# Optimization experiments

Measured on AMD Instinct MI355X. Metric: run time of the kernel, lower is better.

## Reference

```python
import jax, jax.numpy as jnp
import numpy as np
from jax import lax

N_CTX = 65536   # total contexts
B = 512         # samples (segments for attention pooling)
E = 128         # emb_size
H = 128         # rnn_size // 2 (per direction)
T = 9           # path length
SUB_V = 50000
NODE_V = 512
DEC = 320
OUT = 10000
L = N_CTX * 5   # total subtoken occurrences per side


def setup_inputs() -> dict:
    key = jax.random.key(0)
    ks = jax.random.split(key, 24)
    s = 0.05
    d = {}
    d["ll_subtokens"] = jax.random.randint(ks[0], (L,), 0, SUB_V, dtype=jnp.int32)
    d["ll_indices"] = jnp.sort(jax.random.randint(ks[1], (L,), 0, N_CTX, dtype=jnp.int32))
    d["rl_subtokens"] = jax.random.randint(ks[2], (L,), 0, SUB_V, dtype=jnp.int32)
    d["rl_indices"] = jnp.sort(jax.random.randint(ks[3], (L,), 0, N_CTX, dtype=jnp.int32))
    d["paths"] = jax.random.randint(ks[4], (N_CTX, T), 0, NODE_V, dtype=jnp.int32)
    d["indices"] = jnp.sort(jax.random.randint(ks[5], (N_CTX,), 0, B, dtype=jnp.int32))
    d["subtoken_emb"] = jax.random.normal(ks[6], (SUB_V, E), jnp.float32) * s
    d["node_emb"] = jax.random.normal(ks[7], (NODE_V, E), jnp.float32) * s
    d["w_ih_f"] = jax.random.normal(ks[8], (4 * H, E), jnp.float32) * s
    d["w_hh_f"] = jax.random.normal(ks[9], (4 * H, H), jnp.float32) * s
    d["b_ih_f"] = jax.random.normal(ks[10], (4 * H,), jnp.float32) * s
    d["b_hh_f"] = jax.random.normal(ks[11], (4 * H,), jnp.float32) * s
    d["w_ih_b"] = jax.random.normal(ks[12], (4 * H, E), jnp.float32) * s
    d["w_hh_b"] = jax.random.normal(ks[13], (4 * H, H), jnp.float32) * s
    d["b_ih_b"] = jax.random.normal(ks[14], (4 * H,), jnp.float32) * s
    d["b_hh_b"] = jax.random.normal(ks[15], (4 * H,), jnp.float32) * s
    d["fc_w"] = jax.random.normal(ks[16], (DEC, 2 * E + 2 * H), jnp.float32) * s
    d["a"] = jax.random.uniform(ks[17], (DEC,), jnp.float32)  # nn.init.uniform_
    d["out_w"] = jax.random.normal(ks[18], (OUT, DEC), jnp.float32) * s
    d["out_b"] = jax.random.normal(ks[19], (OUT,), jnp.float32) * s
    return d


def _lstm_last_hidden(x, w_ih, w_hh, b_ih, b_hh):
    """x: [T, N, E] -> final hidden state [N, H]. PyTorch gate order i,f,g,o."""
    n = x.shape[1]
    bias = b_ih + b_hh

    def step(carry, xt):
        h, c = carry
        g = xt @ w_ih.T + h @ w_hh.T + bias          # [N, 4H]
        i, f, gg, o = jnp.split(g, 4, axis=-1)
        c = jax.nn.sigmoid(f) * c + jax.nn.sigmoid(i) * jnp.tanh(gg)
        h = jax.nn.sigmoid(o) * jnp.tanh(c)
        return (h, c), None

    init = (jnp.zeros((n, H), x.dtype), jnp.zeros((n, H), x.dtype))
    (h, _), _ = lax.scan(step, init, x)
    return h


def reference(ll_subtokens, ll_indices, rl_subtokens, rl_indices, paths, indices,
              subtoken_emb, node_emb,
              w_ih_f, w_hh_f, b_ih_f, b_hh_f,
              w_ih_b, w_hh_b, b_ih_b, b_hh_b,
              fc_w, a, out_w, out_b):
    # scatter-add subtoken embeddings into per-context leaf embeddings
    ll_emb = jax.ops.segment_sum(subtoken_emb[ll_subtokens], ll_indices, num_segments=N_CTX)
    rl_emb = jax.ops.segment_sum(subtoken_emb[rl_subtokens], rl_indices, num_segments=N_CTX)

    # bidirectional LSTM over path node embeddings; final hidden states
    x = jnp.swapaxes(node_emb[paths], 0, 1)          # [T, N_CTX, E]
    h_f = _lstm_last_hidden(x, w_ih_f, w_hh_f, b_ih_f, b_hh_f)
    h_b = _lstm_last_hidden(x[::-1], w_ih_b, w_hh_b, b_ih_b, b_hh_b)
    path_agg = jnp.concatenate([h_f, h_b], axis=1)   # [N_CTX, 2H]

    ctx = jnp.concatenate([ll_emb, path_agg, rl_emb], axis=1)  # [N_CTX, 2E+2H]
    # dropout is identity in eval mode
    ctx = jnp.tanh(ctx @ fc_w.T)                     # [N_CTX, DEC]

    # segment softmax attention over contexts within each sample
    score = ctx @ a                                  # [N_CTX]
    m = jax.ops.segment_max(score, indices, num_segments=B)
    e = jnp.exp(score - m[indices])
    s = jax.ops.segment_sum(e, indices, num_segments=B)
    w = e / s[indices]
    v = jax.ops.segment_sum(ctx * w[:, None], indices, num_segments=B)  # [B, DEC]

    return v @ out_w.T + out_b                       # [B, OUT]
```

## Files before the change

### kernel.cpp

```cpp
#include <hip/hip_runtime.h>


#define N_CTX_ 65536
#define B_     512
#define E_     128
#define H_     128
#define T_     9
#define DEC_   320
#define OUT_   10000
#define L_     (N_CTX_*5)

typedef __bf16 bf16;
typedef __bf16 bf16x8 __attribute__((ext_vector_type(8)));
typedef __bf16 bf16x4 __attribute__((ext_vector_type(4)));
typedef float  f32x4  __attribute__((ext_vector_type(4)));
typedef float  f32x2  __attribute__((ext_vector_type(2)));
typedef __fp16 f16x2  __attribute__((ext_vector_type(2)));

__device__ __forceinline__ float fast_sig(float x){
  float e = __builtin_amdgcn_exp2f(x * -1.4426950408889634f);
  return __builtin_amdgcn_rcpf(1.0f + e);
}
__device__ __forceinline__ float fast_tanh(float x){
  float e = __builtin_amdgcn_exp2f(x * -2.8853900817779268f);
  return 2.0f * __builtin_amdgcn_rcpf(1.0f + e) - 1.0f;
}
__device__ __forceinline__ int lbound(const int* __restrict__ a, int n, int key){
  int lo = 0, hi = n;
  while (lo < hi){ int mid = (lo + hi) >> 1; if (a[mid] < key) lo = mid + 1; else hi = mid; }
  return lo;
}

__device__ __forceinline__ f32x2 pkmul(f32x2 a, f32x2 b){
  f32x2 d; asm("v_pk_mul_f32 %0, %1, %2" : "=v"(d) : "v"(a), "v"(b)); return d;
}
__device__ __forceinline__ f32x2 pkfma(f32x2 a, f32x2 b, f32x2 c){
  f32x2 d; asm("v_pk_fma_f32 %0, %1, %2, %3" : "=v"(d) : "v"(a), "v"(b), "v"(c)); return d;
}
__device__ __forceinline__ f32x2 pkfma_s(f32x2 a, f32x2 b, f32x2 c){
  f32x2 d; asm("v_pk_fma_f32 %0, %1, %2, %3" : "=v"(d) : "v"(a), "v"(b), "s"(c)); return d;
}

__device__ __forceinline__ f32x4 sig4(f32x4 x){
  const f32x2 S3v = {-2.1081349e-4f, -2.1081349e-4f};
  const f32x2 S2  = { 2.0833333e-3f,  2.0833333e-3f};
  const f32x2 S1  = {-2.0833333e-2f, -2.0833333e-2f};
  const f32x2 S0  = { 0.25f, 0.25f};
  const f32x2 HF  = { 0.5f, 0.5f};
  f32x2 xl = {x[0], x[1]}, xh = {x[2], x[3]};
  f32x2 tl = pkmul(xl, xl), th = pkmul(xh, xh);
  f32x2 pl = pkfma_s(tl, S3v, S2), ph = pkfma_s(th, S3v, S2);
  pl = pkfma_s(pl, tl, S1); ph = pkfma_s(ph, th, S1);
  pl = pkfma_s(pl, tl, S0); ph = pkfma_s(ph, th, S0);
  pl = pkfma_s(xl, pl, HF); ph = pkfma_s(xh, ph, HF);
  return f32x4{pl[0], pl[1], ph[0], ph[1]};
}
__device__ __forceinline__ f32x4 tanh4(f32x4 x){
  const f32x2 C4v = { 0.021869489f,  0.021869489f};
  const f32x2 C3  = {-0.053968254f, -0.053968254f};
  const f32x2 C2  = { 0.13333333f,   0.13333333f};
  const f32x2 C1  = {-0.33333333f,  -0.33333333f};
  const f32x2 C0  = { 1.0f, 1.0f};
  f32x2 xl = {x[0], x[1]}, xh = {x[2], x[3]};
  f32x2 tl = pkmul(xl, xl), th = pkmul(xh, xh);
  f32x2 pl = pkfma_s(tl, C4v, C3), ph = pkfma_s(th, C4v, C3);
  pl = pkfma_s(pl, tl, C2); ph = pkfma_s(ph, th, C2);
  pl = pkfma_s(pl, tl, C1); ph = pkfma_s(ph, th, C1);
  pl = pkfma_s(pl, tl, C0); ph = pkfma_s(ph, th, C0);
  pl = pkmul(xl, pl); ph = pkmul(xh, ph);
  return f32x4{pl[0], pl[1], ph[0], ph[1]};
}
__device__ __forceinline__ f32x4 mul4(f32x4 a, f32x4 b){
  f32x2 l = pkmul(f32x2{a[0],a[1]}, f32x2{b[0],b[1]});
  f32x2 h = pkmul(f32x2{a[2],a[3]}, f32x2{b[2],b[3]});
  return f32x4{l[0], l[1], h[0], h[1]};
}
__device__ __forceinline__ f32x4 fma4(f32x4 a, f32x4 b, f32x4 c){
  f32x2 l = pkfma(f32x2{a[0],a[1]}, f32x2{b[0],b[1]}, f32x2{c[0],c[1]});
  f32x2 h = pkfma(f32x2{a[2],a[3]}, f32x2{b[2],b[3]}, f32x2{c[2],c[3]});
  return f32x4{l[0], l[1], h[0], h[1]};
}

__global__ __launch_bounds__(256) void k_pf(
    const float* __restrict__ nemb,
    const float* __restrict__ wihf, const float* __restrict__ bihf, const float* __restrict__ bhhf,
    const float* __restrict__ wihb, const float* __restrict__ bihb, const float* __restrict__ bhhb,
    bf16* __restrict__ Pf4, bf16* __restrict__ Pb4)
{
  const int node = blockIdx.x, dir = blockIdx.y;
  const float* wih = dir ? wihb : wihf;
  const float* bi  = dir ? bihb : bihf;
  const float* bh  = dir ? bhhb : bhhf;
  bf16* P = dir ? Pb4 : Pf4;
  __shared__ float x[128];
  if (threadIdx.x < 128) x[threadIdx.x] = nemb[node*128 + threadIdx.x];
  __syncthreads();
  const float4* x4 = (const float4*)x;
  #pragma unroll
  for (int jj = 0; jj < 2; ++jj){
    int j = threadIdx.x + jj*256;
    const float4* w4 = (const float4*)(wih + j*128);
    float acc = bi[j] + bh[j];
    #pragma unroll
    for (int k = 0; k < 32; ++k){
      float4 a = w4[k], b = x4[k];
      acc += a.x*b.x + a.y*b.y + a.z*b.z + a.w*b.w;
    }
    int gate = j >> 7, n = (j >> 4) & 7, cc = j & 15;
    int slot = (gate < 2) ? (1 - gate) : gate;
    P[(((size_t)node*16 + cc) << 5) + slot*8 + n] = (bf16)acc;
  }
}

__global__ __launch_bounds__(256) void k_cvt(
    const float* __restrict__ fcw, const float* __restrict__ outw,
    const float* __restrict__ whhf, const float* __restrict__ whhb_,
    const float* __restrict__ semb,
    bf16* __restrict__ fcwb, bf16* __restrict__ outwb,
    bf16* __restrict__ whhfb, bf16* __restrict__ whhbb, bf16* __restrict__ sembb)
{
  size_t i = ((size_t)blockIdx.x*256 + threadIdx.x) * 4;
  const float* src; bf16* dst; size_t off;
  if      (i < 163840)              { src = fcw;   dst = fcwb;  off = i; }
  else if (i < 163840+3200000)      { src = outw;  dst = outwb; off = i - 163840; }
  else if (i < 163840+3200000+65536){ src = whhf;  dst = whhfb; off = i - 3363840; }
  else if (i < 3429376+65536)       { src = whhb_; dst = whhbb; off = i - 3429376; }
  else                              { src = semb;  dst = sembb; off = i - 3494912; }
  float4 v = *(const float4*)(src + off);
  bf16x4 o; o[0]=(bf16)v.x; o[1]=(bf16)v.y; o[2]=(bf16)v.z; o[3]=(bf16)v.w;
  *(bf16x4*)(dst + off) = o;
}

__global__ __launch_bounds__(256) void k_bounds(
    const int* __restrict__ lli, const int* __restrict__ rli,
    int* __restrict__ startL, int* __restrict__ startR)
{
  const int* si = blockIdx.y ? rli : lli;
  int* st = blockIdx.y ? startR : startL;
  int p = blockIdx.x*256 + threadIdx.x;
  if (p > L_) return;
  int cur = (p < L_) ? si[p] : N_CTX_;
  int prv = (p > 0) ? si[p-1] : -1;
  for (int c = prv + 1; c <= cur; ++c) st[c] = p;
}

__global__ __launch_bounds__(256) void k_leaf(
    const int* __restrict__ lls, const int* __restrict__ rls,
    const int* __restrict__ startL, const int* __restrict__ startR,
    const bf16* __restrict__ sembb, bf16* __restrict__ ctx_in)
{
  int u = blockIdx.x*4 + (threadIdx.x >> 6);
  int lane = threadIdx.x & 63;
  int ctx = u >> 1, side = u & 1;
  const int* st  = side ? rls    : lls;
  const int* stt = side ? startR : startL;
  int a = stt[ctx], b = stt[ctx+1];
  float a0 = 0.f, a1 = 0.f;
  for (int p = a; p < b; ++p){
    unsigned w = *(const unsigned*)&sembb[(size_t)st[p]*128 + lane*2];
    a0 += __uint_as_float(w << 16);
    a1 += __uint_as_float(w & 0xffff0000u);
  }
  bf16 r0 = (bf16)a0, r1 = (bf16)a1;
  unsigned pk = ((unsigned)*(unsigned short*)&r1 << 16) | *(unsigned short*)&r0;
  *(unsigned*)&ctx_in[(size_t)ctx*512 + (side ? 384 : 0) + lane*2] = pk;
}

__device__ __forceinline__ void slot_mfma(
    int slot, const bf16* __restrict__ whh, int lo4, int hi4,
    const bf16x8 afr[][4], const int nd[][4], const bf16* __restrict__ P4,
    f32x4 acc[][8])
{
  bf16x8 pv[2][4];
  #pragma unroll
  for (int m = 0; m < 2; ++m)
  #pragma unroll
  for (int r = 0; r < 4; ++r)
    pv[m][r] = *(const bf16x8*)(P4 + (((size_t)nd[m][r]*16 + lo4) << 5) + slot*8);
  #pragma unroll
  for (int m = 0; m < 2; ++m)
  #pragma unroll
  for (int n = 0; n < 8; ++n){
    f32x4 a;
    #pragma unroll
    for (int r = 0; r < 4; ++r){
      unsigned w = ((const unsigned*)&pv[m][r])[n >> 1];
      a[r] = (n & 1) ? __uint_as_float(w & 0xffff0000u) : __uint_as_float(w << 16);
    }
    acc[m][n] = a;
  }
  #pragma unroll
  for (int n = 0; n < 8; ++n)
  #pragma unroll
  for (int kk = 0; kk < 4; ++kk){
    int row = slot*128 + n*16 + lo4;
    bf16x8 bfr = *(const bf16x8*)&whh[row*128 + (((kk*4 + hi4) ^ (row & 15)) << 3)];
    acc[0][n] = __builtin_amdgcn_mfma_f32_16x16x32_bf16(afr[0][kk], bfr, acc[0][n], 0,0,0);
    acc[1][n] = __builtin_amdgcn_mfma_f32_16x16x32_bf16(afr[1][kk], bfr, acc[1][n], 0,0,0);
  }
}

__global__ __launch_bounds__(512, 2) void k_lstm(
    const int* __restrict__ paths,
    const bf16* __restrict__ whhfb, const bf16* __restrict__ whhbb,
    const bf16* __restrict__ Pf4,   const bf16* __restrict__ Pb4,
    bf16* __restrict__ ctx_in)
{
  const int dir = blockIdx.y;
  const bf16* __restrict__ whhg = dir ? whhbb : whhfb;
  const bf16* __restrict__ P4   = dir ? Pb4   : Pf4;
  __shared__ __align__(16) bf16 whh[512*128];
  __shared__ __align__(16) bf16 hlds[8*16*64];
  const int tid = threadIdx.x;
  const int lane = tid & 63, wid = tid >> 6;
  const int lo4 = lane & 15, hi4 = lane >> 4;

  #pragma unroll
  for (int it = 0; it < 16; ++it){
    int i = tid + it*512;
    int srow = i >> 4, c16 = i & 15;
    int gate = srow >> 7, rr = srow & 127;
    int slot = (gate < 2) ? (1 - gate) : gate;
    int drow = slot*128 + rr;
    *(bf16x8*)&whh[drow*128 + ((c16 ^ (drow & 15)) << 3)] =
        *(const bf16x8*)&whhg[srow*128 + c16*8];
  }
  __syncthreads();

  bf16* __restrict__ hbuf = &hlds[wid*1024];
  const int ctx0 = blockIdx.x*256 + wid*32;

  f32x4 c[2][8];
  bf16x8 afr[2][4];
  #pragma unroll
  for (int m = 0; m < 2; ++m){
    #pragma unroll
    for (int n = 0; n < 8; ++n) c[m][n] = f32x4{0.f,0.f,0.f,0.f};
    #pragma unroll
    for (int kk = 0; kk < 4; ++kk) afr[m][kk] = bf16x8{};
  }

  int nd[2][4];
  {
    int tt0 = dir ? (T_-1) : 0;
    #pragma unroll
    for (int m = 0; m < 2; ++m)
    #pragma unroll
    for (int r = 0; r < 4; ++r)
      nd[m][r] = paths[(ctx0 + m*16 + hi4*4 + r)*T_ + tt0];
  }

  #pragma unroll 1
  for (int s = 0; s < T_; ++s){
    int ndn[2][4];
    if (s + 1 < T_){
      int ttn = dir ? (T_-2-s) : (s+1);
      #pragma unroll
      for (int m = 0; m < 2; ++m)
      #pragma unroll
      for (int r = 0; r < 4; ++r)
        ndn[m][r] = paths[(ctx0 + m*16 + hi4*4 + r)*T_ + ttn];
    }
    f32x4 acc[2][8];
    f16x2 iact[2][8][2];

    slot_mfma(0, whh, lo4, hi4, afr, nd, P4, acc);
    #pragma unroll
    for (int m = 0; m < 2; ++m)
    #pragma unroll
    for (int n = 0; n < 8; ++n) c[m][n] = mul4(sig4(acc[m][n]), c[m][n]);

    slot_mfma(1, whh, lo4, hi4, afr, nd, P4, acc);
    #pragma unroll
    for (int m = 0; m < 2; ++m)
    #pragma unroll
    for (int n = 0; n < 8; ++n){
      f32x4 sv = sig4(acc[m][n]);
      iact[m][n][0] = __builtin_amdgcn_cvt_pkrtz(sv[0], sv[1]);
      iact[m][n][1] = __builtin_amdgcn_cvt_pkrtz(sv[2], sv[3]);
    }

    slot_mfma(2, whh, lo4, hi4, afr, nd, P4, acc);
    #pragma unroll
    for (int m = 0; m < 2; ++m)
    #pragma unroll
    for (int n = 0; n < 8; ++n){
      f32x4 ia = {(float)iact[m][n][0][0], (float)iact[m][n][0][1],
                  (float)iact[m][n][1][0], (float)iact[m][n][1][1]};
      c[m][n] = fma4(ia, tanh4(acc[m][n]), c[m][n]);
    }

    slot_mfma(3, whh, lo4, hi4, afr, nd, P4, acc);
    #pragma unroll
    for (int mp = 0; mp < 2; ++mp){
      f32x4 hv[8];
      #pragma unroll
      for (int n = 0; n < 8; ++n) hv[n] = mul4(sig4(acc[mp][n]), tanh4(c[mp][n]));
      if (s < T_-1){
        #pragma unroll
        for (int np = 0; np < 2; ++np){
          #pragma unroll
          for (int n2 = 0; n2 < 4; ++n2)
          #pragma unroll
          for (int r = 0; r < 4; ++r){
            int row = hi4*4 + r;
            int colb = n2*16 + lo4;
            hbuf[row*64 + (((colb >> 3) ^ (row & 7)) << 3) + (colb & 7)] =
                (bf16)hv[np*4 + n2][r];
          }
          #pragma unroll
          for (int kk2 = 0; kk2 < 2; ++kk2)
            afr[mp][np*2 + kk2] =
                *(const bf16x8*)&hbuf[lo4*64 + (((kk2*4 + hi4) ^ (lo4 & 7)) << 3)];
        }
      } else {
        #pragma unroll
        for (int n = 0; n < 8; ++n)
        #pragma unroll
        for (int r = 0; r < 4; ++r)
          ctx_in[(size_t)(ctx0 + mp*16 + hi4*4 + r)*512 + 128 + dir*128 + n*16 + lo4] =
              (bf16)hv[n][r];
      }
    }
    #pragma unroll
    for (int m = 0; m < 2; ++m)
    #pragma unroll
    for (int r = 0; r < 4; ++r) nd[m][r] = ndn[m][r];
  }
}

__global__ __launch_bounds__(256, 2) void k_fc(
    const bf16* __restrict__ ctx_in, const bf16* __restrict__ fcwb,
    const float* __restrict__ avec, bf16* __restrict__ ctxb, float* __restrict__ score)
{
  __shared__ __align__(16) bf16 bsl[320*32];
  const int tid = threadIdx.x, lane = tid & 63, wid = tid >> 6;
  const int lo4 = lane & 15, hi4 = lane >> 4;
  const int rowbase = blockIdx.x*64 + wid*16;
  bf16x8 afr[16];
  #pragma unroll
  for (int kk = 0; kk < 16; ++kk)
    afr[kk] = *(const bf16x8*)&ctx_in[(size_t)(rowbase + lo4)*512 + kk*32 + hi4*8];
  f32x4 acc[20];
  #pragma unroll
  for (int nt = 0; nt < 20; ++nt) acc[nt] = f32x4{0.f,0.f,0.f,0.f};
  #pragma unroll
  for (int kk = 0; kk < 16; ++kk){
    __syncthreads();
    #pragma unroll
    for (int i = 0; i < 5; ++i){
      int cc = tid + i*256;
      int row = cc >> 2, cg = (cc & 3) << 3;
      *(bf16x8*)&bsl[row*32 + (cg ^ ((row & 3) << 3))] =
          *(const bf16x8*)&fcwb[(size_t)row*512 + kk*32 + cg];
    }
    __syncthreads();
    #pragma unroll
    for (int nt = 0; nt < 20; ++nt){
      int row = nt*16 + lo4;
      bf16x8 b = *(const bf16x8*)&bsl[row*32 + ((hi4*8) ^ ((row & 3) << 3))];
      acc[nt] = __builtin_amdgcn_mfma_f32_16x16x32_bf16(afr[kk], b, acc[nt], 0,0,0);
    }
  }
  float sc[4] = {0.f,0.f,0.f,0.f};
  #pragma unroll
  for (int nt = 0; nt < 20; ++nt){
    float av = avec[nt*16 + lo4];
    #pragma unroll
    for (int r = 0; r < 4; ++r){
      float t = fast_tanh(acc[nt][r]);
      ctxb[(size_t)(rowbase + hi4*4 + r)*320 + nt*16 + lo4] = (bf16)t;
      sc[r] += t * av;
    }
  }
  #pragma unroll
  for (int r = 0; r < 4; ++r){
    #pragma unroll
    for (int o = 1; o < 16; o <<= 1) sc[r] += __shfl_xor(sc[r], o, 64);
  }
  if (lo4 == 0){
    #pragma unroll
    for (int r = 0; r < 4; ++r) score[rowbase + hi4*4 + r] = sc[r];
  }
}

__global__ __launch_bounds__(320) void k_attn(
    const int* __restrict__ sidx, const float* __restrict__ score,
    const bf16* __restrict__ ctxb, bf16* __restrict__ vb)
{
  const int b = blockIdx.x, tid = threadIdx.x;
  const int lane = tid & 63, wid = tid >> 6;
  const int lo = lbound(sidx, N_CTX_, b);
  const int hi = lbound(sidx, N_CTX_, b + 1);
  __shared__ float red[16];
  float m = -3.0e38f;
  for (int p = lo + tid; p < hi; p += 320) m = fmaxf(m, score[p]);
  #pragma unroll
  for (int o = 1; o < 64; o <<= 1) m = fmaxf(m, __shfl_xor(m, o, 64));
  if (lane == 0) red[wid] = m;
  __syncthreads();
  m = red[0];
  #pragma unroll
  for (int w = 1; w < 5; ++w) m = fmaxf(m, red[w]);
  float sp = 0.f;
  for (int p = lo + tid; p < hi; p += 320)
    sp += __builtin_amdgcn_exp2f((score[p] - m) * 1.4426950408889634f);
  #pragma unroll
  for (int o = 1; o < 64; o <<= 1) sp += __shfl_xor(sp, o, 64);
  __syncthreads();
  if (lane == 0) red[8 + wid] = sp;
  __syncthreads();
  float ssum = red[8] + red[9] + red[10] + red[11] + red[12];
  float inv = __builtin_amdgcn_rcpf(ssum);
  const float K2 = 1.4426950408889634f;
  float v = 0.f;
// ... 57 lines not shown
      for (int r = 0; r < 4; ++r)
        out[(size_t)(bb + hi4*4 + r)*OUT_ + o] = acc[nt][r] + bias;
    }
  }
}

extern "C" void kernel_launch(void* const* d_in, const int* in_sizes, int n_in,
                              void* d_out, int out_size, void* d_ws, size_t ws_size,
                              hipStream_t stream)
{
  const int*   lls  = (const int*)d_in[0];
  const int*   lli  = (const int*)d_in[1];
  const int*   rls  = (const int*)d_in[2];
  const int*   rli  = (const int*)d_in[3];
  const int*   paths= (const int*)d_in[4];
  const int*   sidx = (const int*)d_in[5];
  const float* semb = (const float*)d_in[6];
  const float* nemb = (const float*)d_in[7];
  const float* wihf = (const float*)d_in[8];
  const float* whhf = (const float*)d_in[9];
  const float* bihf = (const float*)d_in[10];
  const float* bhhf = (const float*)d_in[11];
  const float* wihb = (const float*)d_in[12];
  const float* whhb = (const float*)d_in[13];
  const float* bihb = (const float*)d_in[14];
  const float* bhhb = (const float*)d_in[15];
  const float* fcw  = (const float*)d_in[16];
  const float* avec = (const float*)d_in[17];
  const float* outw = (const float*)d_in[18];
  const float* outb = (const float*)d_in[19];
  float* out = (float*)d_out;

  char* w = (char*)d_ws;
  bf16*  Pf4   = (bf16*)w;  w += (size_t)512*512*2;
  bf16*  Pb4   = (bf16*)w;  w += (size_t)512*512*2;
  bf16*  ctx_in= (bf16*)w;  w += (size_t)N_CTX_*512*2;
  bf16*  ctxb  = (bf16*)w;  w += (size_t)N_CTX_*320*2;
  float* score = (float*)w; w += (size_t)N_CTX_*4;
  bf16*  vb    = (bf16*)w;  w += (size_t)512*320*2;
  bf16*  fcwb  = (bf16*)w;  w += (size_t)320*512*2;
  bf16*  outwb = (bf16*)w;  w += (size_t)OUT_*320*2;
  bf16*  whhfb = (bf16*)w;  w += (size_t)512*128*2;
  bf16*  whhbb = (bf16*)w;  w += (size_t)512*128*2;
  bf16*  sembb = (bf16*)w;  w += (size_t)50000*128*2;
  int*   startL= (int*)w;   w += (size_t)(N_CTX_+16)*4;
  int*   startR= (int*)w;   w += (size_t)(N_CTX_+16)*4;

  k_pf    <<<dim3(512, 2), 256, 0, stream>>>(nemb, wihf, bihf, bhhf, wihb, bihb, bhhb, Pf4, Pb4);
  k_cvt   <<<dim3(9663), 256, 0, stream>>>(fcw, outw, whhf, whhb, semb,
                                           fcwb, outwb, whhfb, whhbb, sembb);
  k_bounds<<<dim3((L_ + 256)/256 + 1, 2), 256, 0, stream>>>(lli, rli, startL, startR);
  k_leaf  <<<dim3(N_CTX_*2/4), 256, 0, stream>>>(lls, rls, startL, startR, sembb, ctx_in);
  k_lstm  <<<dim3(256, 2), 512, 0, stream>>>(paths, whhfb, whhbb, Pf4, Pb4, ctx_in);
  k_fc    <<<dim3(1024), 256, 0, stream>>>(ctx_in, fcwb, avec, ctxb, score);
  k_attn  <<<dim3(512), 320, 0, stream>>>(sidx, score, ctxb, vb);
  k_out   <<<dim3(40, 8), 256, 0, stream>>>(vb, outwb, outb, out);
}
```

Before: 477.9 us.

## Restructure LSTM recurrence to 32x32x16 MFMA with transposed hidden-state layout

The LSTM kernel now computes gates as W_hh * h^T with 32x32x16 bf16 MFMAs. Each lane owns one context, so the path index and P-table rows are loaded per lane, and the hidden state stays in B-fragment registers via a small swizzled LDS round trip. The W_hh slot reordering and swizzle move into the conversion kernel, so the LSTM prologue becomes a plain copy, and P is laid out to match the MFMA output. k_fc also stages its tanh outputs through LDS to write coalesced 16-byte rows, and leaf sums use packed bf16 conversion. The risks are higher register pressure from 16-wide accumulators and LDS bank conflicts.

```diff
diff --git a/kernel.cpp b/kernel.cpp
--- a/kernel.cpp
+++ b/kernel.cpp
@@ -15,12 +15,10 @@
 typedef __bf16 bf16x4 __attribute__((ext_vector_type(4)));
 typedef float  f32x4  __attribute__((ext_vector_type(4)));
 typedef float  f32x2  __attribute__((ext_vector_type(2)));
+typedef float  f32x16 __attribute__((ext_vector_type(16)));
 typedef __fp16 f16x2  __attribute__((ext_vector_type(2)));
-
-__device__ __forceinline__ float fast_sig(float x){
-  float e = __builtin_amdgcn_exp2f(x * -1.4426950408889634f);
-  return __builtin_amdgcn_rcpf(1.0f + e);
-}
+typedef unsigned int u32;
+
 __device__ __forceinline__ float fast_tanh(float x){
   float e = __builtin_amdgcn_exp2f(x * -2.8853900817779268f);
   return 2.0f * __builtin_amdgcn_rcpf(1.0f + e) - 1.0f;
@@ -30,6 +28,11 @@
   while (lo < hi){ int mid = (lo + hi) >> 1; if (a[mid] < key) lo = mid + 1; else hi = mid; }
   return lo;
 }
+__device__ __forceinline__ u32 cvtpk_bf16(float a, float b){
+  u32 d; asm("v_cvt_pk_bf16_f32 %0, %1, %2" : "=v"(d) : "v"(a), "v"(b)); return d;
+}
+__device__ __forceinline__ float bflo(u32 w){ return __uint_as_float(w << 16); }
+__device__ __forceinline__ float bfhi(u32 w){ return __uint_as_float(w & 0xffff0000u); }
 
 __device__ __forceinline__ f32x2 pkmul(f32x2 a, f32x2 b){
   f32x2 d; asm("v_pk_mul_f32 %0, %1, %2" : "=v"(d) : "v"(a), "v"(b)); return d;
@@ -40,7 +43,6 @@
 __device__ __forceinline__ f32x2 pkfma_s(f32x2 a, f32x2 b, f32x2 c){
   f32x2 d; asm("v_pk_fma_f32 %0, %1, %2, %3" : "=v"(d) : "v"(a), "v"(b), "s"(c)); return d;
 }
-
 __device__ __forceinline__ f32x4 sig4(f32x4 x){
   const f32x2 S3v = {-2.1081349e-4f, -2.1081349e-4f};
   const f32x2 S2  = { 2.0833333e-3f,  2.0833333e-3f};
@@ -85,13 +87,13 @@
     const float* __restrict__ nemb,
     const float* __restrict__ wihf, const float* __restrict__ bihf, const float* __restrict__ bhhf,
     const float* __restrict__ wihb, const float* __restrict__ bihb, const float* __restrict__ bhhb,
-    bf16* __restrict__ Pf4, bf16* __restrict__ Pb4)
+    bf16* __restrict__ Pf7, bf16* __restrict__ Pb7)
 {
   const int node = blockIdx.x, dir = blockIdx.y;
   const float* wih = dir ? wihb : wihf;
   const float* bi  = dir ? bihb : bihf;
   const float* bh  = dir ? bhhb : bhhf;
-  bf16* P = dir ? Pb4 : Pf4;
+  bf16* P = dir ? Pb7 : Pf7;
   __shared__ float x[128];
   if (threadIdx.x < 128) x[threadIdx.x] = nemb[node*128 + threadIdx.x];
   __syncthreads();
@@ -106,9 +108,11 @@
       float4 a = w4[k], b = x4[k];
       acc += a.x*b.x + a.y*b.y + a.z*b.z + a.w*b.w;
     }
-    int gate = j >> 7, n = (j >> 4) & 7, cc = j & 15;
+    int gate = j >> 7, jl7 = j & 127;
     int slot = (gate < 2) ? (1 - gate) : gate;
-    P[(((size_t)node*16 + cc) << 5) + slot*8 + n] = (bf16)acc;
+    int nt = jl7 >> 5, jl = jl7 & 31;
+    int q = (jl >> 3) & 3, h1 = (jl >> 2) & 1, r = jl & 3;
+    P[(size_t)node*512 + slot*128 + nt*32 + h1*16 + q*4 + r] = (bf16)acc;
   }
 }
 
@@ -117,18 +121,27 @@
     const float* __restrict__ whhf, const float* __restrict__ whhb_,
     const float* __restrict__ semb,
     bf16* __restrict__ fcwb, bf16* __restrict__ outwb,
-    bf16* __restrict__ whhfb, bf16* __restrict__ whhbb, bf16* __restrict__ sembb)
+    bf16* __restrict__ whhfS, bf16* __restrict__ whhbS, bf16* __restrict__ sembb)
 {
   size_t i = ((size_t)blockIdx.x*256 + threadIdx.x) * 4;
-  const float* src; bf16* dst; size_t off;
+  const float* src; bf16* dst; size_t off; bool scat = false;
   if      (i < 163840)              { src = fcw;   dst = fcwb;  off = i; }
-  else if (i < 163840+3200000)      { src = outw;  dst = outwb; off = i - 163840; }
-  else if (i < 163840+3200000+65536){ src = whhf;  dst = whhfb; off = i - 3363840; }
-  else if (i < 3429376+65536)       { src = whhb_; dst = whhbb; off = i - 3429376; }
+  else if (i < 3363840)             { src = outw;  dst = outwb; off = i - 163840; }
+  else if (i < 3429376)             { src = whhf;  dst = whhfS; off = i - 3363840; scat = true; }
+  else if (i < 3494912)             { src = whhb_; dst = whhbS; off = i - 3429376; scat = true; }
   else                              { src = semb;  dst = sembb; off = i - 3494912; }
   float4 v = *(const float4*)(src + off);
   bf16x4 o; o[0]=(bf16)v.x; o[1]=(bf16)v.y; o[2]=(bf16)v.z; o[3]=(bf16)v.w;
-  *(bf16x4*)(dst + off) = o;
+  size_t d = off;
+  if (scat){
+    int row = (int)(off >> 7), col = (int)(off & 127);
+    int gate = row >> 7, rr = row & 127;
+    int slot = (gate < 2) ? (1 - gate) : gate;
+    int jrow = slot*128 + rr;
+    int cch = col >> 3, jj = col & 7;
+    d = (size_t)jrow*128 + ((cch ^ (jrow & 15)) << 3) + jj;
+  }
+  *(bf16x4*)(dst + d) = o;
 }
 
 __global__ __launch_bounds__(256) void k_bounds(
@@ -161,172 +174,138 @@
     a0 += __uint_as_float(w << 16);
     a1 += __uint_as_float(w & 0xffff0000u);
   }
-  bf16 r0 = (bf16)a0, r1 = (bf16)a1;
-  unsigned pk = ((unsigned)*(unsigned short*)&r1 << 16) | *(unsigned short*)&r0;
-  *(unsigned*)&ctx_in[(size_t)ctx*512 + (side ? 384 : 0) + lane*2] = pk;
-}
-
-__device__ __forceinline__ void slot_mfma(
-    int slot, const bf16* __restrict__ whh, int lo4, int hi4,
-    const bf16x8 afr[][4], const int nd[][4], const bf16* __restrict__ P4,
-    f32x4 acc[][8])
-{
-  bf16x8 pv[2][4];
-  #pragma unroll
-  for (int m = 0; m < 2; ++m)
-  #pragma unroll
-  for (int r = 0; r < 4; ++r)
-    pv[m][r] = *(const bf16x8*)(P4 + (((size_t)nd[m][r]*16 + lo4) << 5) + slot*8);
-  #pragma unroll
-  for (int m = 0; m < 2; ++m)
-  #pragma unroll
-  for (int n = 0; n < 8; ++n){
-    f32x4 a;
-    #pragma unroll
-    for (int r = 0; r < 4; ++r){
-      unsigned w = ((const unsigned*)&pv[m][r])[n >> 1];
-      a[r] = (n & 1) ? __uint_as_float(w & 0xffff0000u) : __uint_as_float(w << 16);
-    }
-    acc[m][n] = a;
-  }
-  #pragma unroll
-  for (int n = 0; n < 8; ++n)
-  #pragma unroll
-  for (int kk = 0; kk < 4; ++kk){
-    int row = slot*128 + n*16 + lo4;
-    bf16x8 bfr = *(const bf16x8*)&whh[row*128 + (((kk*4 + hi4) ^ (row & 15)) << 3)];
-    acc[0][n] = __builtin_amdgcn_mfma_f32_16x16x32_bf16(afr[0][kk], bfr, acc[0][n], 0,0,0);
-    acc[1][n] = __builtin_amdgcn_mfma_f32_16x16x32_bf16(afr[1][kk], bfr, acc[1][n], 0,0,0);
-  }
+  *(unsigned*)&ctx_in[(size_t)ctx*512 + (side ? 384 : 0) + lane*2] = cvtpk_bf16(a0, a1);
 }
 
 __global__ __launch_bounds__(512, 2) void k_lstm(
     const int* __restrict__ paths,
-    const bf16* __restrict__ whhfb, const bf16* __restrict__ whhbb,
-    const bf16* __restrict__ Pf4,   const bf16* __restrict__ Pb4,
+    const bf16* __restrict__ whhfS, const bf16* __restrict__ whhbS,
+    const bf16* __restrict__ Pf7,   const bf16* __restrict__ Pb7,
     bf16* __restrict__ ctx_in)
 {
   const int dir = blockIdx.y;
-  const bf16* __restrict__ whhg = dir ? whhbb : whhfb;
-  const bf16* __restrict__ P4   = dir ? Pb4   : Pf4;
+  const bf16* __restrict__ whhS = dir ? whhbS : whhfS;
+  const bf16* __restrict__ P7   = dir ? Pb7   : Pf7;
   __shared__ __align__(16) bf16 whh[512*128];
-  __shared__ __align__(16) bf16 hlds[8*16*64];
-  const int tid = threadIdx.x;
-  const int lane = tid & 63, wid = tid >> 6;
-  const int lo4 = lane & 15, hi4 = lane >> 4;
-
-  #pragma unroll
-  for (int it = 0; it < 16; ++it){
-    int i = tid + it*512;
-    int srow = i >> 4, c16 = i & 15;
-    int gate = srow >> 7, rr = srow & 127;
-    int slot = (gate < 2) ? (1 - gate) : gate;
-    int drow = slot*128 + rr;
-    *(bf16x8*)&whh[drow*128 + ((c16 ^ (drow & 15)) << 3)] =
-        *(const bf16x8*)&whhg[srow*128 + c16*8];
+  __shared__ __align__(16) bf16 hlds[8*1024];
+  const int tid = threadIdx.x, lane = tid & 63, wid = tid >> 6;
+  const int lo5 = lane & 31, hi1 = lane >> 5;
+
+  {
+    const uint4* s4 = (const uint4*)whhS;
+    uint4* d4 = (uint4*)whh;
+    #pragma unroll
+    for (int it = 0; it < 16; ++it) d4[tid + it*512] = s4[tid + it*512];
   }
   __syncthreads();
 
-  bf16* __restrict__ hbuf = &hlds[wid*1024];
-  const int ctx0 = blockIdx.x*256 + wid*32;
-
-  f32x4 c[2][8];
-  bf16x8 afr[2][4];
-  #pragma unroll
-  for (int m = 0; m < 2; ++m){
-    #pragma unroll
-    for (int n = 0; n < 8; ++n) c[m][n] = f32x4{0.f,0.f,0.f,0.f};
-    #pragma unroll
-    for (int kk = 0; kk < 4; ++kk) afr[m][kk] = bf16x8{};
-  }
-
-  int nd[2][4];
-  {
-    int tt0 = dir ? (T_-1) : 0;
-    #pragma unroll
-    for (int m = 0; m < 2; ++m)
-    #pragma unroll
-    for (int r = 0; r < 4; ++r)
-      nd[m][r] = paths[(ctx0 + m*16 + hi4*4 + r)*T_ + tt0];
-  }
+  char* __restrict__ hb = (char*)&hlds[wid*1024];
+  const int myctx = blockIdx.x*256 + wid*32 + lo5;
+  const int swz = ((lo5 >> 1) & 3) << 4;
+  const int wsel = lo5 & 15;
+
+  f32x16 c[4];
+  bf16x8 bfr[8];
+  #pragma unroll
+  for (int n = 0; n < 4; ++n) c[n] = f32x16{};
+  #pragma unroll
+  for (int k = 0; k < 8; ++k) bfr[k] = bf16x8{};
+
+  int nd = paths[myctx*T_ + (dir ? (T_-1) : 0)];
 
   #pragma unroll 1
   for (int s = 0; s < T_; ++s){
-    int ndn[2][4];
-    if (s + 1 < T_){
-      int ttn = dir ? (T_-2-s) : (s+1);
+    const int ndn = (s+1 < T_) ? paths[myctx*T_ + (dir ? (T_-2-s) : (s+1))] : 0;
+    const bf16* __restrict__ Pp = P7 + ((size_t)nd << 9) + hi1*16;
+
+    f16x2 iact[4][8];
+
+    #pragma unroll
+    for (int slot = 0; slot < 4; ++slot){
+      bf16x8 pv[4][2];
       #pragma unroll
-      for (int m = 0; m < 2; ++m)
+      for (int n = 0; n < 4; ++n){
+        pv[n][0] = *(const bf16x8*)(Pp + slot*128 + n*32);
+        pv[n][1] = *(const bf16x8*)(Pp + slot*128 + n*32 + 8);
+      }
+      f32x16 acc[4];
       #pragma unroll
-      for (int r = 0; r < 4; ++r)
-        ndn[m][r] = paths[(ctx0 + m*16 + hi4*4 + r)*T_ + ttn];
-    }
-    f32x4 acc[2][8];
-    f16x2 iact[2][8][2];
-
-    slot_mfma(0, whh, lo4, hi4, afr, nd, P4, acc);
-    #pragma unroll
-    for (int m = 0; m < 2; ++m)
-    #pragma unroll
-    for (int n = 0; n < 8; ++n) c[m][n] = mul4(sig4(acc[m][n]), c[m][n]);
-
-    slot_mfma(1, whh, lo4, hi4, afr, nd, P4, acc);
-    #pragma unroll
-    for (int m = 0; m < 2; ++m)
-    #pragma unroll
-    for (int n = 0; n < 8; ++n){
-      f32x4 sv = sig4(acc[m][n]);
-      iact[m][n][0] = __builtin_amdgcn_cvt_pkrtz(sv[0], sv[1]);
-      iact[m][n][1] = __builtin_amdgcn_cvt_pkrtz(sv[2], sv[3]);
-    }
-
-    slot_mfma(2, whh, lo4, hi4, afr, nd, P4, acc);
-    #pragma unroll
-    for (int m = 0; m < 2; ++m)
-    #pragma unroll
-    for (int n = 0; n < 8; ++n){
-      f32x4 ia = {(float)iact[m][n][0][0], (float)iact[m][n][0][1],
-                  (float)iact[m][n][1][0], (float)iact[m][n][1][1]};
-      c[m][n] = fma4(ia, tanh4(acc[m][n]), c[m][n]);
-    }
-
-    slot_mfma(3, whh, lo4, hi4, afr, nd, P4, acc);
-    #pragma unroll
-    for (int mp = 0; mp < 2; ++mp){
-      f32x4 hv[8];
+      for (int n = 0; n < 4; ++n) acc[n] = f32x16{};
       #pragma unroll
-      for (int n = 0; n < 8; ++n) hv[n] = mul4(sig4(acc[mp][n]), tanh4(c[mp][n]));
-      if (s < T_-1){
-        #pragma unroll
-        for (int np = 0; np < 2; ++np){
-          #pragma unroll
-          for (int n2 = 0; n2 < 4; ++n2)
-          #pragma unroll
-          for (int r = 0; r < 4; ++r){
-            int row = hi4*4 + r;
-            int colb = n2*16 + lo4;
-            hbuf[row*64 + (((colb >> 3) ^ (row & 7)) << 3) + (colb & 7)] =
-                (bf16)hv[np*4 + n2][r];
-          }
-          #pragma unroll
-          for (int kk2 = 0; kk2 < 2; ++kk2)
-            afr[mp][np*2 + kk2] =
-                *(const bf16x8*)&hbuf[lo4*64 + (((kk2*4 + hi4) ^ (lo4 & 7)) << 3)];
+      for (int kk = 0; kk < 8; ++kk){
+        #pragma unroll
+        for (int n = 0; n < 4; ++n){
+          bf16x8 a = *(const bf16x8*)&whh[(size_t)(slot*128 + n*32 + lo5)*128
+                        + (((kk*2 + hi1) ^ wsel) << 3)];
+          acc[n] = __builtin_amdgcn_mfma_f32_32x32x16_bf16(a, bfr[kk], acc[n], 0,0,0);
+        }
+      }
+      #pragma unroll
+      for (int n = 0; n < 4; ++n){
+        const u32* w0 = (const u32*)&pv[n][0];
+        const u32* w1 = (const u32*)&pv[n][1];
+        #pragma unroll
+        for (int t = 0; t < 4; ++t){
+          acc[n][t*2+0]   += bflo(w0[t]);
+          acc[n][t*2+1]   += bfhi(w0[t]);
+          acc[n][8+t*2+0] += bflo(w1[t]);
+          acc[n][8+t*2+1] += bfhi(w1[t]);
+        }
+      }
+
+      if (slot == 0){
+        #pragma unroll
+        for (int n = 0; n < 4; ++n)
+        #pragma unroll
+        for (int q = 0; q < 4; ++q){
+          f32x4 x = {acc[n][q*4], acc[n][q*4+1], acc[n][q*4+2], acc[n][q*4+3]};
+          f32x4 cv = {c[n][q*4], c[n][q*4+1], c[n][q*4+2], c[n][q*4+3]};
+          f32x4 r = mul4(sig4(x), cv);
+          c[n][q*4]=r[0]; c[n][q*4+1]=r[1]; c[n][q*4+2]=r[2]; c[n][q*4+3]=r[3];
+        }
+      } else if (slot == 1){
+        #pragma unroll
+        for (int n = 0; n < 4; ++n)
+        #pragma unroll
+        for (int q = 0; q < 4; ++q){
+          f32x4 x = {acc[n][q*4], acc[n][q*4+1], acc[n][q*4+2], acc[n][q*4+3]};
+          f32x4 sv = sig4(x);
+          iact[n][q*2]   = __builtin_amdgcn_cvt_pkrtz(sv[0], sv[1]);
+          iact[n][q*2+1] = __builtin_amdgcn_cvt_pkrtz(sv[2], sv[3]);
+        }
+      } else if (slot == 2){
+        #pragma unroll
+        for (int n = 0; n < 4; ++n)
+        #pragma unroll
+        for (int q = 0; q < 4; ++q){
+          f32x4 x = {acc[n][q*4], acc[n][q*4+1], acc[n][q*4+2], acc[n][q*4+3]};
+          f32x4 cv = {c[n][q*4], c[n][q*4+1], c[n][q*4+2], c[n][q*4+3]};
+          f32x4 ia = {(float)iact[n][q*2][0], (float)iact[n][q*2][1],
+                      (float)iact[n][q*2+1][0], (float)iact[n][q*2+1][1]};
+          f32x4 r = fma4(ia, tanh4(x), cv);
+          c[n][q*4]=r[0]; c[n][q*4+1]=r[1]; c[n][q*4+2]=r[2]; c[n][q*4+3]=r[3];
         }
       } else {
         #pragma unroll
-        for (int n = 0; n < 8; ++n)
-        #pragma unroll
-        for (int r = 0; r < 4; ++r)
-          ctx_in[(size_t)(ctx0 + mp*16 + hi4*4 + r)*512 + 128 + dir*128 + n*16 + lo4] =
-              (bf16)hv[n][r];
+        for (int n = 0; n < 4; ++n){
+          #pragma unroll
+          for (int q = 0; q < 4; ++q){
+            f32x4 x = {acc[n][q*4], acc[n][q*4+1], acc[n][q*4+2], acc[n][q*4+3]};
+            f32x4 cv = {c[n][q*4], c[n][q*4+1], c[n][q*4+2], c[n][q*4+3]};
+            f32x4 h = mul4(sig4(x), tanh4(cv));
+            uint2 pk = { cvtpk_bf16(h[0], h[1]), cvtpk_bf16(h[2], h[3]) };
+            *(uint2*)(hb + lo5*64 + (((q*16 + hi1*8)) ^ swz)) = pk;
+          }
+          bfr[2*n]   = *(const bf16x8*)(hb + lo5*64 + (((0*32 + hi1*16)) ^ swz));
+          bfr[2*n+1] = *(const bf16x8*)(hb + lo5*64 + (((1*32 + hi1*16)) ^ swz));
+        }
       }
     }
-    #pragma unroll
-    for (int m = 0; m < 2; ++m)
-    #pragma unroll
-    for (int r = 0; r < 4; ++r) nd[m][r] = ndn[m][r];
-  }
+    nd = ndn;
+  }
+  #pragma unroll
+  for (int kk = 0; kk < 8; ++kk)
+    *(bf16x8*)&ctx_in[(size_t)myctx*512 + 128 + dir*128 + kk*16 + hi1*8] = bfr[kk];
 }
 
 __global__ __launch_bounds__(256, 2) void k_fc(
@@ -334,6 +313,7 @@
     const float* __restrict__ avec, bf16* __restrict__ ctxb, float* __restrict__ score)
 {
   __shared__ __align__(16) bf16 bsl[320*32];
+  __shared__ __align__(16) bf16 obuf[4][16][336];
   const int tid = threadIdx.x, lane = tid & 63, wid = tid >> 6;
   const int lo4 = lane & 15, hi4 = lane >> 4;
   const int rowbase = blockIdx.x*64 + wid*16;
@@ -369,7 +349,7 @@
     #pragma unroll
     for (int r = 0; r < 4; ++r){
       float t = fast_tanh(acc[nt][r]);
-      ctxb[(size_t)(rowbase + hi4*4 + r)*320 + nt*16 + lo4] = (bf16)t;
+      obuf[wid][hi4*4 + r][nt*16 + lo4] = (bf16)t;
       sc[r] += t * av;
     }
   }
@@ -381,6 +361,11 @@
   if (lo4 == 0){
     #pragma unroll
     for (int r = 0; r < 4; ++r) score[rowbase + hi4*4 + r] = sc[r];
+  }
+  #pragma unroll
+  for (int k = 0; k < 10; ++k){
+    bf16x8 v = *(const bf16x8*)&obuf[wid][lo4][(hi4 + 4*k)*8];
+    *(bf16x8*)&ctxb[(size_t)(rowbase + lo4)*320 + (hi4 + 4*k)*8] = v;
   }
 }
 
@@ -504,26 +489,26 @@
   float* out = (float*)d_out;
 
   char* w = (char*)d_ws;
-  bf16*  Pf4   = (bf16*)w;  w += (size_t)512*512*2;
-  bf16*  Pb4   = (bf16*)w;  w += (size_t)512*512*2;
+  bf16*  Pf7   = (bf16*)w;  w += (size_t)512*512*2;
+  bf16*  Pb7   = (bf16*)w;  w += (size_t)512*512*2;
   bf16*  ctx_in= (bf16*)w;  w += (size_t)N_CTX_*512*2;
   bf16*  ctxb  = (bf16*)w;  w += (size_t)N_CTX_*320*2;
   float* score = (float*)w; w += (size_t)N_CTX_*4;
   bf16*  vb    = (bf16*)w;  w += (size_t)512*320*2;
   bf16*  fcwb  = (bf16*)w;  w += (size_t)320*512*2;
   bf16*  outwb = (bf16*)w;  w += (size_t)OUT_*320*2;
-  bf16*  whhfb = (bf16*)w;  w += (size_t)512*128*2;
-  bf16*  whhbb = (bf16*)w;  w += (size_t)512*128*2;
+  bf16*  whhfS = (bf16*)w;  w += (size_t)512*128*2;
+  bf16*  whhbS = (bf16*)w;  w += (size_t)512*128*2;
   bf16*  sembb = (bf16*)w;  w += (size_t)50000*128*2;
   int*   startL= (int*)w;   w += (size_t)(N_CTX_+16)*4;
   int*   startR= (int*)w;   w += (size_t)(N_CTX_+16)*4;
 
-  k_pf    <<<dim3(512, 2), 256, 0, stream>>>(nemb, wihf, bihf, bhhf, wihb, bihb, bhhb, Pf4, Pb4);
+  k_pf    <<<dim3(512, 2), 256, 0, stream>>>(nemb, wihf, bihf, bhhf, wihb, bihb, bhhb, Pf7, Pb7);
   k_cvt   <<<dim3(9663), 256, 0, stream>>>(fcw, outw, whhf, whhb, semb,
-                                           fcwb, outwb, whhfb, whhbb, sembb);
+                                           fcwb, outwb, whhfS, whhbS, sembb);
   k_bounds<<<dim3((L_ + 256)/256 + 1, 2), 256, 0, stream>>>(lli, rli, startL, startR);
   k_leaf  <<<dim3(N_CTX_*2/4), 256, 0, stream>>>(lls, rls, startL, startR, sembb, ctx_in);
-  k_lstm  <<<dim3(256, 2), 512, 0, stream>>>(paths, whhfb, whhbb, Pf4, Pb4, ctx_in);
+  k_lstm  <<<dim3(256, 2), 512, 0, stream>>>(paths, whhfS, whhbS, Pf7, Pb7, ctx_in);
   k_fc    <<<dim3(1024), 256, 0, stream>>>(ctx_in, fcwb, avec, ctxb, score);
   k_attn  <<<dim3(512), 320, 0, stream>>>(sidx, score, ctxb, vb);
   k_out   <<<dim3(40, 8), 256, 0, stream>>>(vb, outwb, outb, out);
```

Result: slower. 646.0 us (+35.2%).

## Restructure LSTM kernel to 16 contexts per wave with 1024-thread blocks

Applied to the files above, without the earlier changes.

The LSTM kernel now gives each wave 16 contexts instead of 32 and runs 16 waves per block (1024 threads), so each block's shared W_hh copy is reused by twice as many waves and fewer registers are needed per wave. The final hidden state is written from the A-fragment registers as vectorized stores instead of scattered bf16 stores. The fc kernel stages its tanh output through LDS so it can write ctxb with 16-byte stores, and leaf sums are packed with v_cvt_pk_bf16_f32. The risks are register spills under the new launch bounds, extra LDS pressure that may limit occupancy, and the larger per-block weight-loading cost.

```diff
diff --git a/kernel.cpp b/kernel.cpp
--- a/kernel.cpp
+++ b/kernel.cpp
@@ -16,11 +16,8 @@
 typedef float  f32x4  __attribute__((ext_vector_type(4)));
 typedef float  f32x2  __attribute__((ext_vector_type(2)));
 typedef __fp16 f16x2  __attribute__((ext_vector_type(2)));
-
-__device__ __forceinline__ float fast_sig(float x){
-  float e = __builtin_amdgcn_exp2f(x * -1.4426950408889634f);
-  return __builtin_amdgcn_rcpf(1.0f + e);
-}
+typedef unsigned int u32;
+
 __device__ __forceinline__ float fast_tanh(float x){
   float e = __builtin_amdgcn_exp2f(x * -2.8853900817779268f);
   return 2.0f * __builtin_amdgcn_rcpf(1.0f + e) - 1.0f;
@@ -30,6 +27,11 @@
   while (lo < hi){ int mid = (lo + hi) >> 1; if (a[mid] < key) lo = mid + 1; else hi = mid; }
   return lo;
 }
+__device__ __forceinline__ u32 cvtpk_bf16(float a, float b){
+  u32 d; asm("v_cvt_pk_bf16_f32 %0, %1, %2" : "=v"(d) : "v"(a), "v"(b)); return d;
+}
+__device__ __forceinline__ float bflo(u32 w){ return __uint_as_float(w << 16); }
+__device__ __forceinline__ float bfhi(u32 w){ return __uint_as_float(w & 0xffff0000u); }
 
 __device__ __forceinline__ f32x2 pkmul(f32x2 a, f32x2 b){
   f32x2 d; asm("v_pk_mul_f32 %0, %1, %2" : "=v"(d) : "v"(a), "v"(b)); return d;
@@ -40,7 +42,6 @@
 __device__ __forceinline__ f32x2 pkfma_s(f32x2 a, f32x2 b, f32x2 c){
   f32x2 d; asm("v_pk_fma_f32 %0, %1, %2, %3" : "=v"(d) : "v"(a), "v"(b), "s"(c)); return d;
 }
-
 __device__ __forceinline__ f32x4 sig4(f32x4 x){
   const f32x2 S3v = {-2.1081349e-4f, -2.1081349e-4f};
   const f32x2 S2  = { 2.0833333e-3f,  2.0833333e-3f};
@@ -122,9 +123,9 @@
   size_t i = ((size_t)blockIdx.x*256 + threadIdx.x) * 4;
   const float* src; bf16* dst; size_t off;
   if      (i < 163840)              { src = fcw;   dst = fcwb;  off = i; }
-  else if (i < 163840+3200000)      { src = outw;  dst = outwb; off = i - 163840; }
-  else if (i < 163840+3200000+65536){ src = whhf;  dst = whhfb; off = i - 3363840; }
-  else if (i < 3429376+65536)       { src = whhb_; dst = whhbb; off = i - 3429376; }
+  else if (i < 3363840)             { src = outw;  dst = outwb; off = i - 163840; }
+  else if (i < 3429376)             { src = whhf;  dst = whhfb; off = i - 3363840; }
+  else if (i < 3494912)             { src = whhb_; dst = whhbb; off = i - 3429376; }
   else                              { src = semb;  dst = sembb; off = i - 3494912; }
   float4 v = *(const float4*)(src + off);
   bf16x4 o; o[0]=(bf16)v.x; o[1]=(bf16)v.y; o[2]=(bf16)v.z; o[3]=(bf16)v.w;
@@ -161,46 +162,27 @@
     a0 += __uint_as_float(w << 16);
     a1 += __uint_as_float(w & 0xffff0000u);
   }
-  bf16 r0 = (bf16)a0, r1 = (bf16)a1;
-  unsigned pk = ((unsigned)*(unsigned short*)&r1 << 16) | *(unsigned short*)&r0;
-  *(unsigned*)&ctx_in[(size_t)ctx*512 + (side ? 384 : 0) + lane*2] = pk;
-}
-
-__device__ __forceinline__ void slot_mfma(
-    int slot, const bf16* __restrict__ whh, int lo4, int hi4,
-    const bf16x8 afr[][4], const int nd[][4], const bf16* __restrict__ P4,
-    f32x4 acc[][8])
-{
-  bf16x8 pv[2][4];
-  #pragma unroll
-  for (int m = 0; m < 2; ++m)
-  #pragma unroll
-  for (int r = 0; r < 4; ++r)
-    pv[m][r] = *(const bf16x8*)(P4 + (((size_t)nd[m][r]*16 + lo4) << 5) + slot*8);
-  #pragma unroll
-  for (int m = 0; m < 2; ++m)
-  #pragma unroll
-  for (int n = 0; n < 8; ++n){
-    f32x4 a;
-    #pragma unroll
-    for (int r = 0; r < 4; ++r){
-      unsigned w = ((const unsigned*)&pv[m][r])[n >> 1];
-      a[r] = (n & 1) ? __uint_as_float(w & 0xffff0000u) : __uint_as_float(w << 16);
-    }
-    acc[m][n] = a;
-  }
-  #pragma unroll
-  for (int n = 0; n < 8; ++n)
-  #pragma unroll
-  for (int kk = 0; kk < 4; ++kk){
-    int row = slot*128 + n*16 + lo4;
-    bf16x8 bfr = *(const bf16x8*)&whh[row*128 + (((kk*4 + hi4) ^ (row & 15)) << 3)];
-    acc[0][n] = __builtin_amdgcn_mfma_f32_16x16x32_bf16(afr[0][kk], bfr, acc[0][n], 0,0,0);
-    acc[1][n] = __builtin_amdgcn_mfma_f32_16x16x32_bf16(afr[1][kk], bfr, acc[1][n], 0,0,0);
-  }
-}
-
-__global__ __launch_bounds__(512, 2) void k_lstm(
+  *(unsigned*)&ctx_in[(size_t)ctx*512 + (side ? 384 : 0) + lane*2] = cvtpk_bf16(a0, a1);
+}
+
+#define LSTM_MM(SLOT) { \
+  bf16x8 pv[4]; \
+  _Pragma("unroll") for (int r = 0; r < 4; ++r) \
+    pv[r] = *(const bf16x8*)(P4 + (((size_t)nd[r]*16 + lo4) << 5) + (SLOT)*8); \
+  _Pragma("unroll") for (int n = 0; n < 8; ++n){ \
+    f32x4 a_; \
+    _Pragma("unroll") for (int r = 0; r < 4; ++r){ \
+      u32 w_ = ((const u32*)&pv[r])[n >> 1]; \
+      a_[r] = (n & 1) ? bfhi(w_) : bflo(w_); } \
+    acc[n] = a_; } \
+  _Pragma("unroll") for (int n = 0; n < 8; ++n) \
+  _Pragma("unroll") for (int kk = 0; kk < 4; ++kk){ \
+    int row_ = (SLOT)*128 + n*16 + lo4; \
+    bf16x8 b_ = *(const bf16x8*)&whh[row_*128 + (((kk*4 + hi4) ^ (row_ & 15)) << 3)]; \
+    acc[n] = __builtin_amdgcn_mfma_f32_16x16x32_bf16(afr[kk], b_, acc[n], 0,0,0); \
+  } }
+
+__global__ __launch_bounds__(1024, 4) void k_lstm(
     const int* __restrict__ paths,
     const bf16* __restrict__ whhfb, const bf16* __restrict__ whhbb,
     const bf16* __restrict__ Pf4,   const bf16* __restrict__ Pb4,
@@ -210,14 +192,14 @@
   const bf16* __restrict__ whhg = dir ? whhbb : whhfb;
   const bf16* __restrict__ P4   = dir ? Pb4   : Pf4;
   __shared__ __align__(16) bf16 whh[512*128];
-  __shared__ __align__(16) bf16 hlds[8*16*64];
+  __shared__ __align__(16) bf16 hlds[16*1024];
   const int tid = threadIdx.x;
   const int lane = tid & 63, wid = tid >> 6;
   const int lo4 = lane & 15, hi4 = lane >> 4;
 
   #pragma unroll
-  for (int it = 0; it < 16; ++it){
-    int i = tid + it*512;
+  for (int it = 0; it < 8; ++it){
+    int i = tid + it*1024;
     int srow = i >> 4, c16 = i & 15;
     int gate = srow >> 7, rr = srow & 127;
     int slot = (gate < 2) ? (1 - gate) : gate;
@@ -228,105 +210,85 @@
   __syncthreads();
 
   bf16* __restrict__ hbuf = &hlds[wid*1024];
-  const int ctx0 = blockIdx.x*256 + wid*32;
-
-  f32x4 c[2][8];
-  bf16x8 afr[2][4];
-  #pragma unroll
-  for (int m = 0; m < 2; ++m){
-    #pragma unroll
-    for (int n = 0; n < 8; ++n) c[m][n] = f32x4{0.f,0.f,0.f,0.f};
-    #pragma unroll
-    for (int kk = 0; kk < 4; ++kk) afr[m][kk] = bf16x8{};
-  }
-
-  int nd[2][4];
+  const int ctx0 = blockIdx.x*256 + wid*16;
+
+  f32x4 c[8];
+  bf16x8 afr[4];
+  #pragma unroll
+  for (int n = 0; n < 8; ++n) c[n] = f32x4{0.f,0.f,0.f,0.f};
+  #pragma unroll
+  for (int kk = 0; kk < 4; ++kk) afr[kk] = bf16x8{};
+
+  int nd[4];
   {
     int tt0 = dir ? (T_-1) : 0;
     #pragma unroll
-    for (int m = 0; m < 2; ++m)
-    #pragma unroll
     for (int r = 0; r < 4; ++r)
-      nd[m][r] = paths[(ctx0 + m*16 + hi4*4 + r)*T_ + tt0];
+      nd[r] = paths[(ctx0 + hi4*4 + r)*T_ + tt0];
   }
 
   #pragma unroll 1
   for (int s = 0; s < T_; ++s){
-    int ndn[2][4];
+    int ndn[4];
     if (s + 1 < T_){
       int ttn = dir ? (T_-2-s) : (s+1);
       #pragma unroll
-      for (int m = 0; m < 2; ++m)
-      #pragma unroll
       for (int r = 0; r < 4; ++r)
-        ndn[m][r] = paths[(ctx0 + m*16 + hi4*4 + r)*T_ + ttn];
-    }
-    f32x4 acc[2][8];
-    f16x2 iact[2][8][2];
-
-    slot_mfma(0, whh, lo4, hi4, afr, nd, P4, acc);
-    #pragma unroll
-    for (int m = 0; m < 2; ++m)
-    #pragma unroll
-    for (int n = 0; n < 8; ++n) c[m][n] = mul4(sig4(acc[m][n]), c[m][n]);
-
-    slot_mfma(1, whh, lo4, hi4, afr, nd, P4, acc);
-    #pragma unroll
-    for (int m = 0; m < 2; ++m)
+        ndn[r] = paths[(ctx0 + hi4*4 + r)*T_ + ttn];
+    }
+    f32x4 acc[8];
+    f16x2 iact[8][2];
+
+    LSTM_MM(0);
+    #pragma unroll
+    for (int n = 0; n < 8; ++n) c[n] = mul4(sig4(acc[n]), c[n]);
+
+    LSTM_MM(1);
     #pragma unroll
     for (int n = 0; n < 8; ++n){
-      f32x4 sv = sig4(acc[m][n]);
-      iact[m][n][0] = __builtin_amdgcn_cvt_pkrtz(sv[0], sv[1]);
-      iact[m][n][1] = __builtin_amdgcn_cvt_pkrtz(sv[2], sv[3]);
-    }
-
-    slot_mfma(2, whh, lo4, hi4, afr, nd, P4, acc);
-    #pragma unroll
-    for (int m = 0; m < 2; ++m)
+      f32x4 sv = sig4(acc[n]);
+      iact[n][0] = __builtin_amdgcn_cvt_pkrtz(sv[0], sv[1]);
+      iact[n][1] = __builtin_amdgcn_cvt_pkrtz(sv[2], sv[3]);
+    }
+
+    LSTM_MM(2);
     #pragma unroll
     for (int n = 0; n < 8; ++n){
-      f32x4 ia = {(float)iact[m][n][0][0], (float)iact[m][n][0][1],
-                  (float)iact[m][n][1][0], (float)iact[m][n][1][1]};
-      c[m][n] = fma4(ia, tanh4(acc[m][n]), c[m][n]);
-    }
-
-    slot_mfma(3, whh, lo4, hi4, afr, nd, P4, acc);
-    #pragma unroll
-    for (int mp = 0; mp < 2; ++mp){
+      f32x4 ia = {(float)iact[n][0][0], (float)iact[n][0][1],
+                  (float)iact[n][1][0], (float)iact[n][1][1]};
+      c[n] = fma4(ia, tanh4(acc[n]), c[n]);
+    }
+
+    LSTM_MM(3);
+    {
       f32x4 hv[8];
       #pragma unroll
-      for (int n = 0; n < 8; ++n) hv[n] = mul4(sig4(acc[mp][n]), tanh4(c[mp][n]));
-      if (s < T_-1){
+      for (int n = 0; n < 8; ++n) hv[n] = mul4(sig4(acc[n]), tanh4(c[n]));
+      #pragma unroll
+      for (int np = 0; np < 2; ++np){
         #pragma unroll
-        for (int np = 0; np < 2; ++np){
-          #pragma unroll
-          for (int n2 = 0; n2 < 4; ++n2)
-          #pragma unroll
-          for (int r = 0; r < 4; ++r){
-            int row = hi4*4 + r;
-            int colb = n2*16 + lo4;
-            hbuf[row*64 + (((colb >> 3) ^ (row & 7)) << 3) + (colb & 7)] =
-                (bf16)hv[np*4 + n2][r];
-          }
-          #pragma unroll
-          for (int kk2 = 0; kk2 < 2; ++kk2)
-            afr[mp][np*2 + kk2] =
-                *(const bf16x8*)&hbuf[lo4*64 + (((kk2*4 + hi4) ^ (lo4 & 7)) << 3)];
+        for (int n2 = 0; n2 < 4; ++n2)
+        #pragma unroll
+        for (int r = 0; r < 4; ++r){
+          int row = hi4*4 + r;
+          int colb = n2*16 + lo4;
+          hbuf[row*64 + (((colb >> 3) ^ (row & 7)) << 3) + (colb & 7)] =
+              (bf16)hv[np*4 + n2][r];
         }
-      } else {
         #pragma unroll
-        for (int n = 0; n < 8; ++n)
-        #pragma unroll
-        for (int r = 0; r < 4; ++r)
-          ctx_in[(size_t)(ctx0 + mp*16 + hi4*4 + r)*512 + 128 + dir*128 + n*16 + lo4] =
-              (bf16)hv[n][r];
+        for (int kk2 = 0; kk2 < 2; ++kk2)
+          afr[np*2 + kk2] =
+              *(const bf16x8*)&hbuf[lo4*64 + (((kk2*4 + hi4) ^ (lo4 & 7)) << 3)];
       }
     }
     #pragma unroll
-    for (int m = 0; m < 2; ++m)
-    #pragma unroll
-    for (int r = 0; r < 4; ++r) nd[m][r] = ndn[m][r];
-  }
+    for (int r = 0; r < 4; ++r) nd[r] = ndn[r];
+  }
+
+  #pragma unroll
+  for (int kk = 0; kk < 4; ++kk)
+    *(bf16x8*)&ctx_in[(size_t)(ctx0 + lo4)*512 + 128 + dir*128 + kk*32 + hi4*8] =
+        afr[kk];
 }
 
 __global__ __launch_bounds__(256, 2) void k_fc(
@@ -334,6 +296,7 @@
     const float* __restrict__ avec, bf16* __restrict__ ctxb, float* __restrict__ score)
 {
   __shared__ __align__(16) bf16 bsl[320*32];
+  __shared__ __align__(16) bf16 obuf[4][16][336];
   const int tid = threadIdx.x, lane = tid & 63, wid = tid >> 6;
   const int lo4 = lane & 15, hi4 = lane >> 4;
   const int rowbase = blockIdx.x*64 + wid*16;
@@ -369,7 +332,7 @@
     #pragma unroll
     for (int r = 0; r < 4; ++r){
       float t = fast_tanh(acc[nt][r]);
-      ctxb[(size_t)(rowbase + hi4*4 + r)*320 + nt*16 + lo4] = (bf16)t;
+      obuf[wid][hi4*4 + r][nt*16 + lo4] = (bf16)t;
       sc[r] += t * av;
     }
   }
@@ -381,6 +344,11 @@
   if (lo4 == 0){
     #pragma unroll
     for (int r = 0; r < 4; ++r) score[rowbase + hi4*4 + r] = sc[r];
+  }
+  #pragma unroll
+  for (int k = 0; k < 10; ++k){
+    bf16x8 v = *(const bf16x8*)&obuf[wid][lo4][(hi4 + 4*k)*8];
+    *(bf16x8*)&ctxb[(size_t)(rowbase + lo4)*320 + (hi4 + 4*k)*8] = v;
   }
 }
 
@@ -523,7 +491,7 @@
                                            fcwb, outwb, whhfb, whhbb, sembb);
   k_bounds<<<dim3((L_ + 256)/256 + 1, 2), 256, 0, stream>>>(lli, rli, startL, startR);
   k_leaf  <<<dim3(N_CTX_*2/4), 256, 0, stream>>>(lls, rls, startL, startR, sembb, ctx_in);
-  k_lstm  <<<dim3(256, 2), 512, 0, stream>>>(paths, whhfb, whhbb, Pf4, Pb4, ctx_in);
+  k_lstm  <<<dim3(256, 2), 1024, 0, stream>>>(paths, whhfb, whhbb, Pf4, Pb4, ctx_in);
   k_fc    <<<dim3(1024), 256, 0, stream>>>(ctx_in, fcwb, avec, ctxb, score);
   k_attn  <<<dim3(512), 320, 0, stream>>>(sidx, score, ctxb, vb);
   k_out   <<<dim3(40, 8), 256, 0, stream>>>(vb, outwb, outb, out);
```

New measurement: 859.0 us. +79.7%, slower.
